# Performance work log

Hardware: AMD Instinct MI355X
Metric: run time of the kernel (lower is better)

## Reference

```python
import jax, jax.numpy as jnp
import numpy as np

B, S, H = 8, 2048, 768
N_SPANS = 512
MAX_SPAN_LEN = 30
WIDTH_VOCAB = 64
N_BIO, N_TYPE, N_SENS = 3, 18, 4
SPAN_DIM = H * 3 + H // 2  # 2688


def setup_inputs() -> dict:
    key = jax.random.key(0)
    ks = jax.random.split(key, 12)
    hidden = jax.random.normal(ks[0], (B, S, H), dtype=jnp.float32)
    # candidate spans: start in [0, S-MAX_SPAN_LEN), width in [1, MAX_SPAN_LEN]
    starts = jax.random.randint(ks[1], (B, N_SPANS), 0, S - MAX_SPAN_LEN)
    widths = jax.random.randint(ks[2], (B, N_SPANS), 1, MAX_SPAN_LEN + 1)
    ends = starts + widths - 1
    candidate_spans = jnp.stack([starts, ends], axis=-1).astype(jnp.int32)  # [B,N,2]
    sc = 0.02
    return {
        "hidden": hidden,
        "candidate_spans": candidate_spans,
        "width_emb": jax.random.normal(ks[3], (WIDTH_VOCAB, H // 2), dtype=jnp.float32) * sc,
        "W_prop": jax.random.normal(ks[4], (H, N_BIO), dtype=jnp.float32) * sc,
        "b_prop": jnp.zeros((N_BIO,), jnp.float32),
        "W_t1": jax.random.normal(ks[5], (SPAN_DIM, H), dtype=jnp.float32) * sc,
        "b_t1": jnp.zeros((H,), jnp.float32),
        "W_t2": jax.random.normal(ks[6], (H, N_TYPE), dtype=jnp.float32) * sc,
        "b_t2": jnp.zeros((N_TYPE,), jnp.float32),
        "W_s1": jax.random.normal(ks[7], (SPAN_DIM + N_TYPE, H), dtype=jnp.float32) * sc,
        "b_s1": jnp.zeros((H,), jnp.float32),
        "W_s2": jax.random.normal(ks[8], (H, N_SENS), dtype=jnp.float32) * sc,
        "b_s2": jnp.zeros((N_SENS,), jnp.float32),
    }


def _span_reprs(hidden, candidate_spans, width_emb):
    # hidden: [B,S,H], candidate_spans: [B,N,2] (all spans valid, 0 <= s <= e < S)
    starts = candidate_spans[..., 0]  # [B,N]
    ends = candidate_spans[..., 1]    # [B,N]
    gather = jax.vmap(lambda h, i: h[i])  # per-batch row gather
    start_h = gather(hidden, starts)  # [B,N,H]
    end_h = gather(hidden, ends)      # [B,N,H]
    # ragged mean-pool via inclusive prefix sums: sum(h[s:e+1]) = P[e+1]-P[s]
    P = jnp.concatenate(
        [jnp.zeros((hidden.shape[0], 1, hidden.shape[2]), hidden.dtype),
         jnp.cumsum(hidden, axis=1)], axis=1)  # [B,S+1,H]
    widths = ends - starts + 1  # [B,N]
    pooled = (gather(P, ends + 1) - gather(P, starts)) / widths[..., None].astype(hidden.dtype)
    width_h = width_emb[jnp.clip(widths, None, WIDTH_VOCAB - 1)]  # [B,N,H//2]
    return jnp.concatenate([start_h, end_h, pooled, width_h], axis=-1)  # [B,N,SPAN_DIM]


def reference(hidden, candidate_spans, width_emb, W_prop, b_prop,
              W_t1, b_t1, W_t2, b_t2, W_s1, b_s1, W_s2, b_s2):
    # proposal head (dropout = identity in eval)
    proposal_logits = hidden @ W_prop + b_prop  # [B,S,3]
    rep = _span_reprs(hidden, candidate_spans, width_emb)  # [B,N,2688]
    t = jax.nn.gelu(rep @ W_t1 + b_t1, approximate=False)
    type_logits = t @ W_t2 + b_t2  # [B,N,18]
    type_probs = jax.nn.softmax(type_logits, axis=-1)
    s_in = jnp.concatenate([rep, type_probs], axis=-1)  # [B,N,2706]
    s = jax.nn.gelu(s_in @ W_s1 + b_s1, approximate=False)
    sensitivity_logits = s @ W_s2 + b_s2  # [B,N,4]
    return proposal_logits, type_logits, sensitivity_logits
```

## Files before the change

kernel.cpp:

```cpp
#include <hip/hip_runtime.h>
#include <hip/hip_bf16.h>
#include <math.h>

#define Bn 8
#define Sn 2048
#define Hn 768
#define NROW 4096
#define SPAN_DIM 2688
#define NBIG 1536
#define NTYPE 18
#define NSENS 4
#define WPAD 24

#define NB_PROP 4096
#define NB_SPAN 4096
#define NB_T    2016
#define NB_SM   156
#define NB_TOTAL (NB_PROP + NB_SPAN + 2 * NB_T + NB_SM)

typedef __attribute__((ext_vector_type(8))) short short8;
typedef __attribute__((ext_vector_type(4))) float floatx4;

__device__ __forceinline__ unsigned short f2bf(float x) {
    __hip_bfloat16 h = __float2bfloat16(x);
    return *reinterpret_cast<unsigned short*>(&h);
}

__device__ __forceinline__ float bfu(unsigned short u) {
    union { float f; unsigned int i; } v;
    v.i = ((unsigned int)u) << 16;
    return v.f;
}

__device__ __forceinline__ void glds16(const void* g, void* l) {
    __builtin_amdgcn_global_load_lds(
        (const __attribute__((address_space(1))) unsigned int*)g,
        (__attribute__((address_space(3))) unsigned int*)l, 16, 0, 0);
}

__device__ __forceinline__ float gelu_exact(float v) {
    return 0.5f * v * (1.f + erff(v * 0.70710678118654752f));
}

__global__ __launch_bounds__(256) void pre_kernel(
    const float* __restrict__ hidden, const int* __restrict__ spans,
    const float* __restrict__ wemb,
    const float* __restrict__ Wp, const float* __restrict__ bp,
    const float* __restrict__ Wt1, const float* __restrict__ Ws1,
    const float* __restrict__ Wt2, const float* __restrict__ Ws2,
    float* __restrict__ out_prop, unsigned short* __restrict__ rep,
    unsigned short* __restrict__ WbigT,
    unsigned short* __restrict__ Wt2bf, unsigned short* __restrict__ Wtailbf,
    unsigned short* __restrict__ Ws2bf)
{
    __shared__ float tile[32][33];
    int id = blockIdx.x;
    int tid = threadIdx.x;

    if (id < NB_PROP) {
        int wave = tid >> 6, lane = tid & 63;
        int row = id * 4 + wave;
        const float4* h4 = (const float4*)(hidden + (size_t)row * Hn);
        float a0 = 0.f, a1 = 0.f, a2 = 0.f;
#pragma unroll
        for (int i = 0; i < 3; ++i) {
            int kc = i * 64 + lane;
            float4 h = h4[kc];
            const float* w = Wp + kc * 12;
            a0 += h.x * w[0] + h.y * w[3] + h.z * w[6] + h.w * w[9];
            a1 += h.x * w[1] + h.y * w[4] + h.z * w[7] + h.w * w[10];
            a2 += h.x * w[2] + h.y * w[5] + h.z * w[8] + h.w * w[11];
        }
#pragma unroll
        for (int off = 32; off; off >>= 1) {
            a0 += __shfl_xor(a0, off);
            a1 += __shfl_xor(a1, off);
            a2 += __shfl_xor(a2, off);
        }
        if (lane < 3) {
            float v = (lane == 0 ? a0 : (lane == 1 ? a1 : a2)) + bp[lane];
            out_prop[row * 3 + lane] = v;
        }
        return;
    }
    id -= NB_PROP;
    if (id < NB_SPAN) {
        if (tid >= 192) return;
        int n = id;
        int b = n >> 9;
        int s = spans[n * 2 + 0];
        int e = spans[n * 2 + 1];
        int w = e - s + 1;
        const float4* hb4 = (const float4*)(hidden + (size_t)b * Sn * Hn);
        unsigned short* r = rep + (size_t)n * SPAN_DIM;
        float inv_w = 1.0f / (float)w;

        float4 sv = hb4[(size_t)s * 192 + tid];
        float4 ev = hb4[(size_t)e * 192 + tid];
        float4 p0 = make_float4(0.f, 0.f, 0.f, 0.f), p1 = p0, p2 = p0, p3 = p0;
        int rr = s;
        for (; rr + 3 <= e; rr += 4) {
            float4 h0 = hb4[(size_t)(rr + 0) * 192 + tid];
            float4 h1 = hb4[(size_t)(rr + 1) * 192 + tid];
            float4 h2 = hb4[(size_t)(rr + 2) * 192 + tid];
            float4 h3 = hb4[(size_t)(rr + 3) * 192 + tid];
            p0.x += h0.x; p0.y += h0.y; p0.z += h0.z; p0.w += h0.w;
            p1.x += h1.x; p1.y += h1.y; p1.z += h1.z; p1.w += h1.w;
            p2.x += h2.x; p2.y += h2.y; p2.z += h2.z; p2.w += h2.w;
            p3.x += h3.x; p3.y += h3.y; p3.z += h3.z; p3.w += h3.w;
        }
        for (; rr <= e; ++rr) {
            float4 h = hb4[(size_t)rr * 192 + tid];
            p0.x += h.x; p0.y += h.y; p0.z += h.z; p0.w += h.w;
        }
        float4 pv;
        pv.x = ((p0.x + p1.x) + (p2.x + p3.x)) * inv_w;
        pv.y = ((p0.y + p1.y) + (p2.y + p3.y)) * inv_w;
        pv.z = ((p0.z + p1.z) + (p2.z + p3.z)) * inv_w;
        pv.w = ((p0.w + p1.w) + (p2.w + p3.w)) * inv_w;

        *(ushort4*)&r[tid * 4] =
            make_ushort4(f2bf(sv.x), f2bf(sv.y), f2bf(sv.z), f2bf(sv.w));
        *(ushort4*)&r[Hn + tid * 4] =
            make_ushort4(f2bf(ev.x), f2bf(ev.y), f2bf(ev.z), f2bf(ev.w));
        *(ushort4*)&r[2 * Hn + tid * 4] =
            make_ushort4(f2bf(pv.x), f2bf(pv.y), f2bf(pv.z), f2bf(pv.w));
        if (tid < 96) {
            int wi = w > 63 ? 63 : w;
            float4 wv = ((const float4*)wemb)[wi * 96 + tid];
            *(ushort4*)&r[3 * Hn + tid * 4] =
                make_ushort4(f2bf(wv.x), f2bf(wv.y), f2bf(wv.z), f2bf(wv.w));
        }
        return;
    }
    id -= NB_SPAN;
    if (id < 2 * NB_T) {
        int z = id / NB_T, l = id - z * NB_T;
        const float* W = (z == 0) ? Wt1 : Ws1;
        unsigned short* Wt = WbigT + (size_t)z * Hn * SPAN_DIM;
        int k0 = (l % 84) * 32, n0 = (l / 84) * 32;
        int tx = tid & 31, ty = tid >> 5;
#pragma unroll
        for (int i = 0; i < 32; i += 8)
            tile[ty + i][tx] = W[(size_t)(k0 + ty + i) * Hn + n0 + tx];
        __syncthreads();
#pragma unroll
        for (int i = 0; i < 32; i += 8)
            Wt[(size_t)(n0 + ty + i) * SPAN_DIM + k0 + tx] = f2bf(tile[tx][ty + i]);
        return;
    }
    id -= 2 * NB_T;
    {
        int idx = id * 256 + tid;
        const int N1 = Hn * WPAD;
        const int N2 = 2 * N1;
        const int N3 = N2 + Hn * NSENS;
        if (idx < N1) {
            int k = idx / WPAD, o = idx - k * WPAD;
            Wt2bf[idx] = (o < NTYPE) ? f2bf(Wt2[k * NTYPE + o]) : 0;
        } else if (idx < N2) {
            int j = idx - N1;
            int k = j / WPAD, o = j - k * WPAD;
            Wtailbf[j] = (o < NTYPE) ? f2bf(Ws1[(size_t)(SPAN_DIM + o) * Hn + k]) : 0;
        } else if (idx < N3) {
            int j = idx - N2;
            Ws2bf[j] = f2bf(Ws2[j]);
        }
    }
}

__global__ __launch_bounds__(256, 2) void gemm_fused(
    const unsigned short* __restrict__ A,
    const unsigned short* __restrict__ Bt,
    const float* __restrict__ bt1, const float* __restrict__ bs1,
    unsigned short* __restrict__ obuf)
{
    const int BK = 64;
    __shared__ unsigned short As[128 * BK];
    __shared__ unsigned short Bs[128 * BK];

    int tid = threadIdx.x, wave = tid >> 6, lane = tid & 63;
    int m0 = blockIdx.x * 128, n0 = blockIdx.y * 128;

    int wr = (wave >> 1) * 64;
    int wc = (wave & 1) * 64;
    int fr = lane & 15;
    int fc = lane >> 4;

    const unsigned short* gA[4];
    const unsigned short* gB[4];
#pragma unroll
    for (int j = 0; j < 4; ++j) {
        int d = tid + j * 256;
        int r = d >> 3, c = (d & 7) ^ (r & 7);
        gA[j] = A + (size_t)(m0 + r) * SPAN_DIM + c * 8;
        gB[j] = Bt + (size_t)(n0 + r) * SPAN_DIM + c * 8;
    }
    int off[4];
#pragma unroll
    for (int j = 0; j < 4; ++j) off[j] = j * 2048 + wave * 512;

    floatx4 acc[4][4] = {};

    for (int k0 = 0; k0 < SPAN_DIM; k0 += BK) {
        glds16(gA[0] + k0, &As[off[0]]);
        glds16(gA[1] + k0, &As[off[1]]);
        glds16(gA[2] + k0, &As[off[2]]);
        glds16(gA[3] + k0, &As[off[3]]);
        glds16(gB[0] + k0, &Bs[off[0]]);
        glds16(gB[1] + k0, &Bs[off[1]]);
        glds16(gB[2] + k0, &Bs[off[2]]);
        glds16(gB[3] + k0, &Bs[off[3]]);
        __syncthreads();

#pragma unroll
        for (int half = 0; half < 2; ++half) {
            int cb = half * 4 + fc;
            short8 af[4], bf[4];
#pragma unroll
            for (int i = 0; i < 4; ++i) {
                int r = wr + i * 16 + fr;
                af[i] = *(const short8*)&As[((r << 3) | (cb ^ (r & 7))) * 8];
            }
#pragma unroll
            for (int i = 0; i < 4; ++i) {
                int r = wc + i * 16 + fr;
                bf[i] = *(const short8*)&Bs[((r << 3) | (cb ^ (r & 7))) * 8];
            }
#pragma unroll
            for (int mi = 0; mi < 4; ++mi)
#pragma unroll
                for (int ni = 0; ni < 4; ++ni)
                    acc[mi][ni] = __builtin_amdgcn_mfma_f32_16x16x32_bf16(
                        af[mi], bf[ni], acc[mi][ni], 0, 0, 0);
        }
        __syncthreads();
    }

    bool isT = (n0 < Hn);
    const float* bias = isT ? bt1 : (bs1 - Hn);
    int cr = (lane >> 4) * 4;
#pragma unroll
    for (int mi = 0; mi < 4; ++mi) {
#pragma unroll
        for (int ni = 0; ni < 4; ++ni) {
            int col = n0 + wc + ni * 16 + fr;
            float bv = bias[col];
#pragma unroll
            for (int r = 0; r < 4; ++r) {
                int row = m0 + wr + mi * 16 + cr + r;
                float v = acc[mi][ni][r] + bv;
                if (isT) v = gelu_exact(v);
                obuf[(size_t)row * NBIG + col] = f2bf(v);
            }
        }
    }
}

__global__ __launch_bounds__(256) void heads_kernel(
    const unsigned short* __restrict__ obuf, const unsigned short* __restrict__ Wt2bf,
    const float* __restrict__ bt2, const unsigned short* __restrict__ Wtailbf,
    const unsigned short* __restrict__ Ws2bf, const float* __restrict__ bs2,
    float* __restrict__ out_type, float* __restrict__ out_sens)
{
    int wave = threadIdx.x >> 6, lane = threadIdx.x & 63;
    int row = blockIdx.x * 4 + wave;
    const ushort4* tr4 = (const ushort4*)(obuf + (size_t)row * NBIG);

    float acc[NTYPE] = {};
#pragma unroll
    for (int i = 0; i < 3; ++i) {
        ushort4 tc = tr4[lane + i * 64];
        float tv[4] = {bfu(tc.x), bfu(tc.y), bfu(tc.z), bfu(tc.w)};
#pragma unroll
        for (int j = 0; j < 4; ++j) {
            int k = (lane + i * 64) * 4 + j;
            const unsigned short* wp = Wt2bf + (size_t)k * WPAD;
            short8 w0 = *(const short8*)wp;
            short8 w1 = *(const short8*)(wp + 8);
            ushort4 w2 = *(const ushort4*)(wp + 16);
#pragma unroll
            for (int o = 0; o < 8; ++o) acc[o] += tv[j] * bfu((unsigned short)w0[o]);
#pragma unroll
            for (int o = 0; o < 8; ++o) acc[8 + o] += tv[j] * bfu((unsigned short)w1[o]);
            acc[16] += tv[j] * bfu(w2.x);
            acc[17] += tv[j] * bfu(w2.y);
        }
    }
#pragma unroll
    for (int o = 0; o < NTYPE; ++o)
#pragma unroll
        for (int off = 32; off; off >>= 1) acc[o] += __shfl_xor(acc[o], off);

    float mx = -1e30f;
#pragma unroll
    for (int o = 0; o < NTYPE; ++o) { acc[o] += bt2[o]; mx = fmaxf(mx, acc[o]); }
    {
        float lv = 0.f;
#pragma unroll
        for (int o = 0; o < NTYPE; ++o) lv = (lane == o) ? acc[o] : lv;
        if (lane < NTYPE) out_type[row * NTYPE + lane] = lv;
    }
    float pr[NTYPE], sum = 0.f;
#pragma unroll
    for (int o = 0; o < NTYPE; ++o) { pr[o] = expf(acc[o] - mx); sum += pr[o]; }
    float inv = 1.f / sum;
#pragma unroll
    for (int o = 0; o < NTYPE; ++o) pr[o] *= inv;

    const ushort4* sp4 = (const ushort4*)(obuf + (size_t)row * NBIG + Hn);
    float acc2[NSENS] = {};
#pragma unroll
    for (int i = 0; i < 3; ++i) {
        ushort4 sc = sp4[lane + i * 64];
        float sv[4] = {bfu(sc.x), bfu(sc.y), bfu(sc.z), bfu(sc.w)};
#pragma unroll
        for (int j = 0; j < 4; ++j) {
            int k = (lane + i * 64) * 4 + j;
            const unsigned short* wt = Wtailbf + (size_t)k * WPAD;
            short8 a0 = *(const short8*)wt;
            short8 a1 = *(const short8*)(wt + 8);
            ushort4 a2 = *(const ushort4*)(wt + 16);
            float tl = 0.f;
#pragma unroll
            for (int o = 0; o < 8; ++o) tl += pr[o] * bfu((unsigned short)a0[o]);
#pragma unroll
            for (int o = 0; o < 8; ++o) tl += pr[8 + o] * bfu((unsigned short)a1[o]);
            tl += pr[16] * bfu(a2.x) + pr[17] * bfu(a2.y);
            float v = gelu_exact(sv[j] + tl);
            ushort4 wv = *(const ushort4*)(Ws2bf + (size_t)k * NSENS);
            acc2[0] += v * bfu(wv.x);
            acc2[1] += v * bfu(wv.y);
            acc2[2] += v * bfu(wv.z);
            acc2[3] += v * bfu(wv.w);
        }
    }
#pragma unroll
    for (int o = 0; o < NSENS; ++o)
#pragma unroll
        for (int off = 32; off; off >>= 1) acc2[o] += __shfl_xor(acc2[o], off);
    {
        float lv = 0.f;
#pragma unroll
        for (int o = 0; o < NSENS; ++o) lv = (lane == o) ? (acc2[o] + bs2[o]) : lv;
        if (lane < NSENS) out_sens[row * NSENS + lane] = lv;
    }
}

extern "C" void kernel_launch(void* const* d_in, const int* in_sizes, int n_in,
                              void* d_out, int out_size, void* d_ws, size_t ws_size,
                              hipStream_t stream)
{
    const float* hidden = (const float*)d_in[0];
    const int*   spans  = (const int*)d_in[1];
    const float* wemb   = (const float*)d_in[2];
    const float* Wp     = (const float*)d_in[3];
    const float* bp     = (const float*)d_in[4];
    const float* Wt1    = (const float*)d_in[5];
    const float* bt1    = (const float*)d_in[6];
    const float* Wt2    = (const float*)d_in[7];
    const float* bt2    = (const float*)d_in[8];
    const float* Ws1    = (const float*)d_in[9];
    const float* bs1    = (const float*)d_in[10];
    const float* Ws2    = (const float*)d_in[11];
    const float* bs2    = (const float*)d_in[12];

    float* out      = (float*)d_out;
    float* out_prop = out;
    float* out_type = out + Bn * Sn * 3;
    float* out_sens = out_type + NROW * NTYPE;

    unsigned short* rep  = (unsigned short*)d_ws;
    unsigned short* obuf = rep + (size_t)NROW * SPAN_DIM;
    unsigned short* WbigT = obuf + (size_t)NROW * NBIG;
    unsigned short* Wt2bf   = WbigT + (size_t)NBIG * SPAN_DIM;
    unsigned short* Wtailbf = Wt2bf + Hn * WPAD;
    unsigned short* Ws2bf   = Wtailbf + Hn * WPAD;

    pre_kernel<<<NB_TOTAL, 256, 0, stream>>>(
        hidden, spans, wemb, Wp, bp, Wt1, Ws1, Wt2, Ws2,
        out_prop, rep, WbigT, Wt2bf, Wtailbf, Ws2bf);

    dim3 gg(NROW / 128, NBIG / 128);
    gemm_fused<<<gg, 256, 0, stream>>>(rep, WbigT, bt1, bs1, obuf);

    heads_kernel<<<NROW / 4, 256, 0, stream>>>(
        obuf, Wt2bf, bt2, Wtailbf, Ws2bf, bs2, out_type, out_sens);
}
```

Measured before the change: 222.5 us.

## Switch GEMM to 128x64 tiles with intra-block split-K across waves

The fused GEMM tile shrinks from 128x128 to 128x64 output, doubling the grid to 768 blocks. The four waves now split as two M halves times two K halves, and the partial sums are reduced through shared memory before the bias, GELU and bf16 store. Launch bounds rise to three blocks per CU. The aim is better occupancy and CU load balance on a small grid. The cost is lower arithmetic intensity (A tiles are reloaded twice as often) and an extra shared-memory reduction pass.

```diff
diff --git a/kernel.cpp b/kernel.cpp
--- a/kernel.cpp
+++ b/kernel.cpp
@@ -169,89 +169,107 @@
     }
 }
 
-__global__ __launch_bounds__(256, 2) void gemm_fused(
+__global__ __launch_bounds__(256, 3) void gemm_fused(
     const unsigned short* __restrict__ A,
     const unsigned short* __restrict__ Bt,
     const float* __restrict__ bt1, const float* __restrict__ bs1,
     unsigned short* __restrict__ obuf)
 {
     const int BK = 64;
-    __shared__ unsigned short As[128 * BK];
-    __shared__ unsigned short Bs[128 * BK];
+    __shared__ __align__(16) unsigned char smem[32768];
+    unsigned short* As = (unsigned short*)smem;
+    unsigned short* Bs = As + 128 * BK;
 
     int tid = threadIdx.x, wave = tid >> 6, lane = tid & 63;
-    int m0 = blockIdx.x * 128, n0 = blockIdx.y * 128;
-
-    int wr = (wave >> 1) * 64;
-    int wc = (wave & 1) * 64;
+    int m0 = blockIdx.x * 128, n0 = blockIdx.y * 64;
+
+    int mh = wave >> 1;
+    int kh = wave & 1;
     int fr = lane & 15;
-    int fc = lane >> 4;
+    int fq = lane >> 4;
 
     const unsigned short* gA[4];
-    const unsigned short* gB[4];
 #pragma unroll
     for (int j = 0; j < 4; ++j) {
         int d = tid + j * 256;
         int r = d >> 3, c = (d & 7) ^ (r & 7);
         gA[j] = A + (size_t)(m0 + r) * SPAN_DIM + c * 8;
+    }
+    const unsigned short* gB[2];
+#pragma unroll
+    for (int j = 0; j < 2; ++j) {
+        int d = tid + j * 256;
+        int r = d >> 3, c = (d & 7) ^ (r & 7);
         gB[j] = Bt + (size_t)(n0 + r) * SPAN_DIM + c * 8;
     }
-    int off[4];
-#pragma unroll
-    for (int j = 0; j < 4; ++j) off[j] = j * 2048 + wave * 512;
+    int offA[4], offB[2];
+#pragma unroll
+    for (int j = 0; j < 4; ++j) offA[j] = j * 2048 + wave * 512;
+#pragma unroll
+    for (int j = 0; j < 2; ++j) offB[j] = j * 2048 + wave * 512;
 
     floatx4 acc[4][4] = {};
+    int cb = kh * 4 + fq;
 
     for (int k0 = 0; k0 < SPAN_DIM; k0 += BK) {
-        glds16(gA[0] + k0, &As[off[0]]);
-        glds16(gA[1] + k0, &As[off[1]]);
-        glds16(gA[2] + k0, &As[off[2]]);
-        glds16(gA[3] + k0, &As[off[3]]);
-        glds16(gB[0] + k0, &Bs[off[0]]);
-        glds16(gB[1] + k0, &Bs[off[1]]);
-        glds16(gB[2] + k0, &Bs[off[2]]);
-        glds16(gB[3] + k0, &Bs[off[3]]);
+        glds16(gA[0] + k0, &As[offA[0]]);
+        glds16(gA[1] + k0, &As[offA[1]]);
+        glds16(gA[2] + k0, &As[offA[2]]);
+        glds16(gA[3] + k0, &As[offA[3]]);
+        glds16(gB[0] + k0, &Bs[offB[0]]);
+        glds16(gB[1] + k0, &Bs[offB[1]]);
         __syncthreads();
 
-#pragma unroll
-        for (int half = 0; half < 2; ++half) {
-            int cb = half * 4 + fc;
-            short8 af[4], bf[4];
-#pragma unroll
-            for (int i = 0; i < 4; ++i) {
-                int r = wr + i * 16 + fr;
-                af[i] = *(const short8*)&As[((r << 3) | (cb ^ (r & 7))) * 8];
-            }
-#pragma unroll
-            for (int i = 0; i < 4; ++i) {
-                int r = wc + i * 16 + fr;
-                bf[i] = *(const short8*)&Bs[((r << 3) | (cb ^ (r & 7))) * 8];
-            }
-#pragma unroll
-            for (int mi = 0; mi < 4; ++mi)
-#pragma unroll
-                for (int ni = 0; ni < 4; ++ni)
-                    acc[mi][ni] = __builtin_amdgcn_mfma_f32_16x16x32_bf16(
-                        af[mi], bf[ni], acc[mi][ni], 0, 0, 0);
-        }
+        short8 af[4], bf[4];
+#pragma unroll
+        for (int i = 0; i < 4; ++i) {
+            int r = mh * 64 + i * 16 + fr;
+            af[i] = *(const short8*)&As[((r << 3) | (cb ^ (r & 7))) * 8];
+        }
+#pragma unroll
+        for (int i = 0; i < 4; ++i) {
+            int r = i * 16 + fr;
+            bf[i] = *(const short8*)&Bs[((r << 3) | (cb ^ (r & 7))) * 8];
+        }
+#pragma unroll
+        for (int mi = 0; mi < 4; ++mi)
+#pragma unroll
+            for (int ni = 0; ni < 4; ++ni)
+                acc[mi][ni] = __builtin_amdgcn_mfma_f32_16x16x32_bf16(
+                    af[mi], bf[ni], acc[mi][ni], 0, 0, 0);
         __syncthreads();
     }
 
-    bool isT = (n0 < Hn);
-    const float* bias = isT ? bt1 : (bs1 - Hn);
+    float* red = (float*)smem;
+    float* myred = red + mh * 4096;
     int cr = (lane >> 4) * 4;
-#pragma unroll
-    for (int mi = 0; mi < 4; ++mi) {
-#pragma unroll
-        for (int ni = 0; ni < 4; ++ni) {
-            int col = n0 + wc + ni * 16 + fr;
-            float bv = bias[col];
-#pragma unroll
-            for (int r = 0; r < 4; ++r) {
-                int row = m0 + wr + mi * 16 + cr + r;
-                float v = acc[mi][ni][r] + bv;
-                if (isT) v = gelu_exact(v);
-                obuf[(size_t)row * NBIG + col] = f2bf(v);
+    if (kh == 1) {
+#pragma unroll
+        for (int mi = 0; mi < 4; ++mi)
+#pragma unroll
+            for (int ni = 0; ni < 4; ++ni)
+#pragma unroll
+                for (int r = 0; r < 4; ++r)
+                    myred[(mi * 16 + cr + r) * 64 + ni * 16 + fr] = acc[mi][ni][r];
+    }
+    __syncthreads();
+    if (kh == 0) {
+        bool isT = (n0 < Hn);
+        const float* bias = isT ? bt1 : (bs1 - Hn);
+#pragma unroll
+        for (int mi = 0; mi < 4; ++mi) {
+#pragma unroll
+            for (int ni = 0; ni < 4; ++ni) {
+                int col = n0 + ni * 16 + fr;
+                float bv = bias[col];
+#pragma unroll
+                for (int r = 0; r < 4; ++r) {
+                    int row = m0 + mh * 64 + mi * 16 + cr + r;
+                    float v = acc[mi][ni][r] +
+                              myred[(mi * 16 + cr + r) * 64 + ni * 16 + fr] + bv;
+                    if (isT) v = gelu_exact(v);
+                    obuf[(size_t)row * NBIG + col] = f2bf(v);
+                }
             }
         }
     }
@@ -381,7 +399,7 @@
         hidden, spans, wemb, Wp, bp, Wt1, Ws1, Wt2, Ws2,
         out_prop, rep, WbigT, Wt2bf, Wtailbf, Ws2bf);
 
-    dim3 gg(NROW / 128, NBIG / 128);
+    dim3 gg(NROW / 128, NBIG / 64);
     gemm_fused<<<gg, 256, 0, stream>>>(rep, WbigT, bt1, bs1, obuf);
 
     heads_kernel<<<NROW / 4, 256, 0, stream>>>(
```

Measured after the change: 217.8 us. -2.1%, faster.
